# Kernel optimization log

Hardware: AMD Instinct MI355X
Metric: run time of the kernel (lower is better)

## Reference

```python
import jax, jax.numpy as jnp
import numpy as np

N_NODES = 100000


def setup_inputs() -> dict:
    key = jax.random.key(0)
    k1, k2, k3, k4, k5, k6 = jax.random.split(key, 6)
    n_edges = 1600000
    in_f, out_f = 64, 64
    x = jax.random.normal(k1, (N_NODES, in_f), dtype=jnp.float32)
    edge_row = jax.random.randint(k2, (n_edges,), 0, N_NODES, dtype=jnp.int32)
    edge_col = jax.random.randint(k3, (n_edges,), 0, N_NODES, dtype=jnp.int32)
    edge_val = jax.random.uniform(k4, (n_edges,), dtype=jnp.float32)
    stdv = 1.0 / np.sqrt(out_f)
    weight = jax.random.uniform(k5, (in_f, out_f), dtype=jnp.float32, minval=-stdv, maxval=stdv)
    bias = jax.random.uniform(k6, (out_f,), dtype=jnp.float32, minval=-stdv, maxval=stdv)
    return {"x": x, "edge_row": edge_row, "edge_col": edge_col,
            "edge_val": edge_val, "weight": weight, "bias": bias}


def reference(x, edge_row, edge_col, edge_val, weight, bias):
    # spmm: support[i] = sum_{e: row[e]==i} val[e] * x[col[e]]
    msgs = edge_val[:, None] * x[edge_col]              # [E, in_f]
    support = jax.ops.segment_sum(msgs, edge_row, num_segments=N_NODES)  # [N, in_f]
    out = support @ weight + bias                       # [N, out_f]
    # row-wise L2 normalize (no eps, matching torch.norm division)
    norm = jnp.linalg.norm(out, axis=1, keepdims=True)  # [N, 1]
    return out / norm
```

## Files before the change

kernel.cpp:

```cpp
#include <hip/hip_runtime.h>

#define N_NODES 100000
#define FDIM 64
#define BROWS 128
#define NBUCK ((N_NODES + BROWS - 1) / BROWS)
#define EDGES_PER_BLK 8192
#define BCAP 3072

#define WS_BBASE_OFF (656u * 1024u)
#define WS_BTOT_OFF  (672u * 1024u)
#define WS_CV_OFF    (1024u * 1024u)
#define WS_XH_OFF    (14u * 1024u * 1024u)

__device__ __forceinline__ unsigned short f2bf(float f) {
    unsigned int u = __float_as_uint(f);
    return (unsigned short)((u + 0x7FFFu + ((u >> 16) & 1u)) >> 16);
}
__device__ __forceinline__ float bf2f(unsigned short h) {
    return __uint_as_float((unsigned int)h << 16);
}

__global__ __launch_bounds__(256) void spmm_atomic(
    const float* __restrict__ x, const int* __restrict__ erow,
    const int* __restrict__ ecol, const float* __restrict__ eval,
    float* __restrict__ out, int n_edges)
{
    int tid = blockIdx.x * 256 + threadIdx.x;
    int e = tid >> 4, l = tid & 15;
    if (e >= n_edges) return;
    int row = erow[e], col = ecol[e];
    float v = eval[e];
    const float4 xv = *reinterpret_cast<const float4*>(x + (size_t)col * FDIM + l * 4);
    float* dst = out + (size_t)row * FDIM + l * 4;
    unsafeAtomicAdd(dst + 0, v * xv.x);
    unsafeAtomicAdd(dst + 1, v * xv.y);
    unsafeAtomicAdd(dst + 2, v * xv.z);
    unsafeAtomicAdd(dst + 3, v * xv.w);
}

__global__ __launch_bounds__(256) void gemm_xw(
    const float* __restrict__ x, const float* __restrict__ W,
    unsigned short* __restrict__ yh)
{
    __shared__ float4 Wl[64][16];
    __shared__ float  s[4][4][68];

    const int t = threadIdx.x;
    for (int i = t; i < 64 * 16; i += 256)
        ((float4*)Wl)[i] = ((const float4*)W)[i];

    const int wid  = t >> 6;
    const int lane = t & 63;
    const int sub  = lane >> 4;
    const int l    = lane & 15;
    const long base = (long)blockIdx.x * 16 + wid * 4;

    float4 sv = *reinterpret_cast<const float4*>(x + base * FDIM + lane * 4);
    *reinterpret_cast<float4*>(&s[wid][lane >> 4][(lane & 15) * 4]) = sv;
    __syncthreads();

    float4 acc = {0.f, 0.f, 0.f, 0.f};
    const float* srow = s[wid][sub];
    #pragma unroll
    for (int k = 0; k < FDIM; ++k) {
        const float a = srow[k];
        const float4 w = Wl[k][l];
        acc.x += a * w.x; acc.y += a * w.y; acc.z += a * w.z; acc.w += a * w.w;
    }
    ushort4 h;
    h.x = f2bf(acc.x); h.y = f2bf(acc.y); h.z = f2bf(acc.z); h.w = f2bf(acc.w);
    *reinterpret_cast<ushort4*>(yh + (size_t)(base + sub) * FDIM + l * 4) = h;
}

__global__ __launch_bounds__(1024) void count_blocks(
    const int* __restrict__ erow, int* __restrict__ cnts,
    int n_edges, int nblk)
{
    __shared__ int cnt[NBUCK];
    const int blk = blockIdx.x, t = threadIdx.x;
    for (int i = t; i < NBUCK; i += 1024) cnt[i] = 0;
    __syncthreads();
    const int beg = blk * EDGES_PER_BLK;
    const int end = min(beg + EDGES_PER_BLK, n_edges);
    for (int i = beg + t; i < end; i += 1024)
        atomicAdd(&cnt[erow[i] >> 7], 1);
    __syncthreads();
    for (int b = t; b < NBUCK; b += 1024)
        cnts[b * nblk + blk] = cnt[b];
}

__global__ __launch_bounds__(256) void scan_within_bucket(
    int* __restrict__ cnts, int* __restrict__ btot, int nblk)
{
    __shared__ int ssum[256];
    const int b = blockIdx.x, t = threadIdx.x;
    const int c = (t < nblk) ? cnts[b * nblk + t] : 0;
    ssum[t] = c;
    __syncthreads();
    for (int off = 1; off < 256; off <<= 1) {
        int v = (t >= off) ? ssum[t - off] : 0;
        __syncthreads();
        ssum[t] += v;
        __syncthreads();
    }
    if (t < nblk) cnts[b * nblk + t] = ssum[t] - c;
    if (t == 255) btot[b] = ssum[255];
}

__global__ __launch_bounds__(1024) void scan_btot(
    const int* __restrict__ btot, int* __restrict__ bbase, int n_edges)
{
    __shared__ int ssum[1024];
    const int t = threadIdx.x;
    const int v0 = (t < NBUCK) ? btot[t] : 0;
    ssum[t] = v0;
    __syncthreads();
    for (int off = 1; off < 1024; off <<= 1) {
        int v = (t >= off) ? ssum[t - off] : 0;
        __syncthreads();
        ssum[t] += v;
        __syncthreads();
    }
    if (t < NBUCK) bbase[t] = ssum[t] - v0;
    if (t == 0) bbase[NBUCK] = n_edges;
}

__global__ __launch_bounds__(1024) void bin_pass2(
    const int* __restrict__ erow, const int* __restrict__ ecol,
    const float* __restrict__ eval, const int* __restrict__ cnts,
    const int* __restrict__ bbase, int2* __restrict__ cvbin,
    int n_edges, int nblk)
{
    __shared__ int cur[NBUCK];
    const int blk = blockIdx.x, t = threadIdx.x;
    for (int b = t; b < NBUCK; b += 1024)
        cur[b] = bbase[b] + cnts[b * nblk + blk];
    __syncthreads();
    const int beg = blk * EDGES_PER_BLK;
    const int end = min(beg + EDGES_PER_BLK, n_edges);
    for (int i = beg + t; i < end; i += 1024) {
        int r = erow[i];
        int b = r >> 7;
        int pos = atomicAdd(&cur[b], 1);
        cvbin[pos] = make_int2(ecol[i] | ((r & 127) << 20), __float_as_int(eval[i]));
    }
}

__global__ __launch_bounds__(256) void sort_bucket(
    const int* __restrict__ bbase, int2* __restrict__ cvbin,
    int* __restrict__ endoff)
{
    __shared__ int2 se[BCAP];
    __shared__ int  hcnt[BROWS];
    __shared__ int  tmp[BROWS];
    __shared__ int  hoff[BROWS];
    const int b = blockIdx.x, t = threadIdx.x;
    const int beg = bbase[b];
    const int end = bbase[b + 1];
    const int n = end - beg;

    for (int i = t; i < n; i += 256) se[i] = cvbin[beg + i];
    if (t < BROWS) hcnt[t] = 0;
    __syncthreads();

    for (int i = t; i < n; i += 256) atomicAdd(&hcnt[se[i].x >> 20], 1);
    __syncthreads();

    if (t < BROWS) tmp[t] = hcnt[t];
    __syncthreads();
    for (int off = 1; off < BROWS; off <<= 1) {
        int val = (t < BROWS && t >= off) ? tmp[t - off] : 0;
        __syncthreads();
        if (t < BROWS) tmp[t] += val;
        __syncthreads();
    }
    if (t < BROWS) hoff[t] = tmp[t] - hcnt[t];
    __syncthreads();

    for (int i = t; i < n; i += 256) {
        int2 e = se[i];
        int pos = atomicAdd(&hoff[e.x >> 20], 1);
        cvbin[beg + pos] = e;
    }
    __syncthreads();

    if (t < BROWS) {
        int row = b * BROWS + t;
        if (row < N_NODES) endoff[row] = beg + hoff[t];
    }
}

__global__ __launch_bounds__(256) void spmm_csr(
    const float* __restrict__ x, const int* __restrict__ endoff,
    const int2* __restrict__ cv, float* __restrict__ out)
{
    const int wave = (blockIdx.x * 256 + threadIdx.x) >> 6;
    if (wave >= N_NODES) return;
    const int lane = threadIdx.x & 63;
    const int sub = lane >> 4, l = lane & 15;
    const int r = wave;
    const int beg = (r == 0) ? 0 : endoff[r - 1];
    const int end = endoff[r];

    float4 acc = {0.f, 0.f, 0.f, 0.f};
    int it = beg + sub;
    for (; it + 12 < end; it += 16) {
        const int2 ea = cv[it];
        const int2 eb = cv[it + 4];
        const int2 ec = cv[it + 8];
        const int2 ed = cv[it + 12];
        const float4 xa = *reinterpret_cast<const float4*>(x + (size_t)(ea.x & 0xFFFFF) * FDIM + l * 4);
        const float4 xb = *reinterpret_cast<const float4*>(x + (size_t)(eb.x & 0xFFFFF) * FDIM + l * 4);
        const float4 xc = *reinterpret_cast<const float4*>(x + (size_t)(ec.x & 0xFFFFF) * FDIM + l * 4);
        const float4 xd = *reinterpret_cast<const float4*>(x + (size_t)(ed.x & 0xFFFFF) * FDIM + l * 4);
        const float va = __int_as_float(ea.y);
        const float vb = __int_as_float(eb.y);
        const float vc = __int_as_float(ec.y);
        const float vd = __int_as_float(ed.y);
        acc.x += va * xa.x; acc.y += va * xa.y; acc.z += va * xa.z; acc.w += va * xa.w;
        acc.x += vb * xb.x; acc.y += vb * xb.y; acc.z += vb * xb.z; acc.w += vb * xb.w;
        acc.x += vc * xc.x; acc.y += vc * xc.y; acc.z += vc * xc.z; acc.w += vc * xc.w;
        acc.x += vd * xd.x; acc.y += vd * xd.y; acc.z += vd * xd.z; acc.w += vd * xd.w;
    }
    for (; it < end; it += 4) {
        const int2 e = cv[it];
        const float v = __int_as_float(e.y);
        const float4 xv = *reinterpret_cast<const float4*>(x + (size_t)(e.x & 0xFFFFF) * FDIM + l * 4);
        acc.x += v * xv.x; acc.y += v * xv.y; acc.z += v * xv.z; acc.w += v * xv.w;
    }
    #pragma unroll
    for (int off = 16; off < 64; off <<= 1) {
        acc.x += __shfl_xor(acc.x, off);
        acc.y += __shfl_xor(acc.y, off);
        acc.z += __shfl_xor(acc.z, off);
        acc.w += __shfl_xor(acc.w, off);
    }
    if (sub == 0)
        *reinterpret_cast<float4*>(out + (size_t)r * FDIM + l * 4) = acc;
}

__global__ __launch_bounds__(256) void spmm_fused(
    const unsigned short* __restrict__ yh, const int* __restrict__ endoff,
    const int2* __restrict__ cv, const float* __restrict__ bias,
    float* __restrict__ out)
{
    const int sg = (blockIdx.x * 256 + threadIdx.x) >> 4;
    if (sg >= N_NODES) return;
    const int l = threadIdx.x & 15;
    const int beg = (sg == 0) ? 0 : endoff[sg - 1];
    const int end = endoff[sg];

    float4 acc = {0.f, 0.f, 0.f, 0.f};
    int it = beg;
    for (; it + 3 < end; it += 4) {
        const int2 ea = cv[it];
        const int2 eb = cv[it + 1];
        const int2 ec = cv[it + 2];
        const int2 ed = cv[it + 3];
        const ushort4 xa = *reinterpret_cast<const ushort4*>(yh + (size_t)(ea.x & 0xFFFFF) * FDIM + l * 4);
        const ushort4 xb = *reinterpret_cast<const ushort4*>(yh + (size_t)(eb.x & 0xFFFFF) * FDIM + l * 4);
        const ushort4 xc = *reinterpret_cast<const ushort4*>(yh + (size_t)(ec.x & 0xFFFFF) * FDIM + l * 4);
        const ushort4 xd = *reinterpret_cast<const ushort4*>(yh + (size_t)(ed.x & 0xFFFFF) * FDIM + l * 4);
        const float va = __int_as_float(ea.y);
        const float vb = __int_as_float(eb.y);
        const float vc = __int_as_float(ec.y);
        const float vd = __int_as_float(ed.y);
        acc.x += va * bf2f(xa.x); acc.y += va * bf2f(xa.y); acc.z += va * bf2f(xa.z); acc.w += va * bf2f(xa.w);
        acc.x += vb * bf2f(xb.x); acc.y += vb * bf2f(xb.y); acc.z += vb * bf2f(xb.z); acc.w += vb * bf2f(xb.w);
        acc.x += vc * bf2f(xc.x); acc.y += vc * bf2f(xc.y); acc.z += vc * bf2f(xc.z); acc.w += vc * bf2f(xc.w);
        acc.x += vd * bf2f(xd.x); acc.y += vd * bf2f(xd.y); acc.z += vd * bf2f(xd.z); acc.w += vd * bf2f(xd.w);
    }
    for (; it < end; ++it) {
        const int2 e = cv[it];
        const float v = __int_as_float(e.y);
        const ushort4 xv = *reinterpret_cast<const ushort4*>(yh + (size_t)(e.x & 0xFFFFF) * FDIM + l * 4);
        acc.x += v * bf2f(xv.x); acc.y += v * bf2f(xv.y); acc.z += v * bf2f(xv.z); acc.w += v * bf2f(xv.w);
    }

    const float4 b = *reinterpret_cast<const float4*>(bias + l * 4);
    acc.x += b.x; acc.y += b.y; acc.z += b.z; acc.w += b.w;

    float p = acc.x * acc.x + acc.y * acc.y + acc.z * acc.z + acc.w * acc.w;
    #pragma unroll
    for (int off = 1; off < 16; off <<= 1)
        p += __shfl_xor(p, off);
    const float inv = 1.0f / sqrtf(p);
    acc.x *= inv; acc.y *= inv; acc.z *= inv; acc.w *= inv;

    *reinterpret_cast<float4*>(out + (size_t)sg * FDIM + l * 4) = acc;
}

__global__ __launch_bounds__(256) void gemm_norm(
    float* __restrict__ io, const float* __restrict__ W,
    const float* __restrict__ bias)
{
    __shared__ float4 Wl[64][16];
    __shared__ float4 bl[16];
    __shared__ float  s[4][4][68];

    const int t = threadIdx.x;
    for (int i = t; i < 64 * 16; i += 256)
        ((float4*)Wl)[i] = ((const float4*)W)[i];
    if (t < 16) bl[t] = ((const float4*)bias)[t];

    const int wid  = t >> 6;
    const int lane = t & 63;
    const int sub  = lane >> 4;
    const int l    = lane & 15;
    const long base = (long)blockIdx.x * 16 + wid * 4;

    float4 sv = *reinterpret_cast<const float4*>(io + base * FDIM + lane * 4);
    *reinterpret_cast<float4*>(&s[wid][lane >> 4][(lane & 15) * 4]) = sv;
    __syncthreads();

    float4 acc = {0.f, 0.f, 0.f, 0.f};
    const float* srow = s[wid][sub];
    #pragma unroll
    for (int k = 0; k < FDIM; ++k) {
        const float a = srow[k];
        const float4 w = Wl[k][l];
        acc.x += a * w.x; acc.y += a * w.y; acc.z += a * w.z; acc.w += a * w.w;
    }
    const float4 b = bl[l];
    acc.x += b.x; acc.y += b.y; acc.z += b.z; acc.w += b.w;

    float p = acc.x*acc.x + acc.y*acc.y + acc.z*acc.z + acc.w*acc.w;
    #pragma unroll
    for (int off = 1; off < 16; off <<= 1)
        p += __shfl_xor(p, off);
    const float inv = 1.0f / sqrtf(p);
    acc.x *= inv; acc.y *= inv; acc.z *= inv; acc.w *= inv;

    *reinterpret_cast<float4*>(io + (base + sub) * FDIM + l * 4) = acc;
}

extern "C" void kernel_launch(void* const* d_in, const int* in_sizes, int n_in,
                              void* d_out, int out_size, void* d_ws, size_t ws_size,
                              hipStream_t stream) {
    const float* x    = (const float*)d_in[0];
    const int*   erow = (const int*)d_in[1];
    const int*   ecol = (const int*)d_in[2];
    const float* eval = (const float*)d_in[3];
    const float* W    = (const float*)d_in[4];
    const float* bias = (const float*)d_in[5];
    float* out = (float*)d_out;
    const int n_edges = in_sizes[1];

    const int nblk = (n_edges + EDGES_PER_BLK - 1) / EDGES_PER_BLK;
    const size_t need = (size_t)WS_CV_OFF + (size_t)n_edges * sizeof(int2);
    const size_t need_bf16 = (size_t)WS_XH_OFF + (size_t)N_NODES * FDIM * sizeof(short);
    const bool cnts_fit =
        (size_t)NBUCK * nblk * sizeof(int) <= WS_BBASE_OFF && nblk <= 256;

    if (ws_size >= need && cnts_fit) {
        int*  cnts   = (int*)d_ws;
        int*  endoff = (int*)d_ws;
        int*  bbase  = (int*)((char*)d_ws + WS_BBASE_OFF);
        int*  btot   = (int*)((char*)d_ws + WS_BTOT_OFF);
        int2* cvbin  = (int2*)((char*)d_ws + WS_CV_OFF);
        unsigned short* yh = (unsigned short*)((char*)d_ws + WS_XH_OFF);
        const bool use_bf16 = (ws_size >= need_bf16);

        if (use_bf16)
            gemm_xw<<<N_NODES / 16, 256, 0, stream>>>(x, W, yh);
        count_blocks<<<nblk, 1024, 0, stream>>>(erow, cnts, n_edges, nblk);
        scan_within_bucket<<<NBUCK, 256, 0, stream>>>(cnts, btot, nblk);
        scan_btot<<<1, 1024, 0, stream>>>(btot, bbase, n_edges);
        bin_pass2<<<nblk, 1024, 0, stream>>>(erow, ecol, eval, cnts, bbase, cvbin,
                                             n_edges, nblk);
        sort_bucket<<<NBUCK, 256, 0, stream>>>(bbase, cvbin, endoff);
        if (use_bf16) {
            spmm_fused<<<((N_NODES * 16) + 255) / 256, 256, 0, stream>>>(
                yh, endoff, cvbin, bias, out);
        } else {
            spmm_csr<<<(N_NODES + 3) / 4, 256, 0, stream>>>(x, endoff, cvbin, out);
            gemm_norm<<<N_NODES / 16, 256, 0, stream>>>(out, W, bias);
        }
    } else {
        hipMemsetAsync(out, 0, (size_t)N_NODES * FDIM * sizeof(float), stream);
        long threads = (long)n_edges * 16;
        spmm_atomic<<<(int)((threads + 255) / 256), 256, 0, stream>>>(
            x, erow, ecol, eval, out, n_edges);
        gemm_norm<<<N_NODES / 16, 256, 0, stream>>>(out, W, bias);
    }
}
```

Before: 102.7 us.

## Fuse bucket sort into SpMM kernel with 64-row buckets held in LDS

Merges the per-bucket counting sort and the bf16 SpMM/bias/normalize kernel into one kernel. Each bucket's sorted edges stay in shared memory instead of being written back to global memory and reread, and the per-row end-offset array is dropped. Buckets shrink to 64 rows (BCAP 1536) and the edge-count blocks grow to 16384 edges, so scan_btot now handles two buckets per thread. A slow linear-scan fallback covers buckets that overflow shared memory, and occupancy and parallelism now depend on only 1563 blocks doing 4 rows per 16-lane group.

```diff
diff --git a/kernel.cpp b/kernel.cpp
--- a/kernel.cpp
+++ b/kernel.cpp
@@ -2,10 +2,10 @@
 
 #define N_NODES 100000
 #define FDIM 64
-#define BROWS 128
+#define BROWS 64
 #define NBUCK ((N_NODES + BROWS - 1) / BROWS)
-#define EDGES_PER_BLK 8192
-#define BCAP 3072
+#define EDGES_PER_BLK 16384
+#define BCAP 1536
 
 #define WS_BBASE_OFF (656u * 1024u)
 #define WS_BTOT_OFF  (672u * 1024u)
@@ -83,7 +83,7 @@
     const int beg = blk * EDGES_PER_BLK;
     const int end = min(beg + EDGES_PER_BLK, n_edges);
     for (int i = beg + t; i < end; i += 1024)
-        atomicAdd(&cnt[erow[i] >> 7], 1);
+        atomicAdd(&cnt[erow[i] >> 6], 1);
     __syncthreads();
     for (int b = t; b < NBUCK; b += 1024)
         cnts[b * nblk + blk] = cnt[b];
@@ -112,8 +112,11 @@
 {
     __shared__ int ssum[1024];
     const int t = threadIdx.x;
-    const int v0 = (t < NBUCK) ? btot[t] : 0;
-    ssum[t] = v0;
+    const int i0 = 2 * t, i1 = 2 * t + 1;
+    const int v0 = (i0 < NBUCK) ? btot[i0] : 0;
+    const int v1 = (i1 < NBUCK) ? btot[i1] : 0;
+    const int s = v0 + v1;
+    ssum[t] = s;
     __syncthreads();
     for (int off = 1; off < 1024; off <<= 1) {
         int v = (t >= off) ? ssum[t - off] : 0;
@@ -121,7 +124,9 @@
         ssum[t] += v;
         __syncthreads();
     }
-    if (t < NBUCK) bbase[t] = ssum[t] - v0;
+    int base = ssum[t] - s;
+    if (i0 < NBUCK) bbase[i0] = base;
+    if (i1 < NBUCK) bbase[i1] = base + v0;
     if (t == 0) bbase[NBUCK] = n_edges;
 }
 
@@ -140,154 +145,113 @@
     const int end = min(beg + EDGES_PER_BLK, n_edges);
     for (int i = beg + t; i < end; i += 1024) {
         int r = erow[i];
-        int b = r >> 7;
+        int b = r >> 6;
         int pos = atomicAdd(&cur[b], 1);
-        cvbin[pos] = make_int2(ecol[i] | ((r & 127) << 20), __float_as_int(eval[i]));
-    }
-}
-
-__global__ __launch_bounds__(256) void sort_bucket(
-    const int* __restrict__ bbase, int2* __restrict__ cvbin,
-    int* __restrict__ endoff)
+        cvbin[pos] = make_int2(ecol[i] | ((r & 63) << 20), __float_as_int(eval[i]));
+    }
+}
+
+__global__ __launch_bounds__(256) void sort_spmm(
+    const int* __restrict__ bbase, const int2* __restrict__ cvbin,
+    const unsigned short* __restrict__ yh, const float* __restrict__ bias,
+    float* __restrict__ out)
 {
     __shared__ int2 se[BCAP];
     __shared__ int  hcnt[BROWS];
-    __shared__ int  tmp[BROWS];
-    __shared__ int  hoff[BROWS];
+    __shared__ int  scn[BROWS];
+    __shared__ int  rowbeg[BROWS];
+    __shared__ int  cur[BROWS];
+
     const int b = blockIdx.x, t = threadIdx.x;
     const int beg = bbase[b];
     const int end = bbase[b + 1];
     const int n = end - beg;
-
-    for (int i = t; i < n; i += 256) se[i] = cvbin[beg + i];
+    const bool fits = (n <= BCAP);
+
     if (t < BROWS) hcnt[t] = 0;
     __syncthreads();
 
-    for (int i = t; i < n; i += 256) atomicAdd(&hcnt[se[i].x >> 20], 1);
-    __syncthreads();
-
-    if (t < BROWS) tmp[t] = hcnt[t];
-    __syncthreads();
-    for (int off = 1; off < BROWS; off <<= 1) {
-        int val = (t < BROWS && t >= off) ? tmp[t - off] : 0;
-        __syncthreads();
-        if (t < BROWS) tmp[t] += val;
-        __syncthreads();
-    }
-    if (t < BROWS) hoff[t] = tmp[t] - hcnt[t];
-    __syncthreads();
-
-    for (int i = t; i < n; i += 256) {
-        int2 e = se[i];
-        int pos = atomicAdd(&hoff[e.x >> 20], 1);
-        cvbin[beg + pos] = e;
-    }
-    __syncthreads();
-
-    if (t < BROWS) {
-        int row = b * BROWS + t;
-        if (row < N_NODES) endoff[row] = beg + hoff[t];
-    }
-}
-
-__global__ __launch_bounds__(256) void spmm_csr(
-    const float* __restrict__ x, const int* __restrict__ endoff,
-    const int2* __restrict__ cv, float* __restrict__ out)
-{
-    const int wave = (blockIdx.x * 256 + threadIdx.x) >> 6;
-    if (wave >= N_NODES) return;
-    const int lane = threadIdx.x & 63;
-    const int sub = lane >> 4, l = lane & 15;
-    const int r = wave;
-    const int beg = (r == 0) ? 0 : endoff[r - 1];
-    const int end = endoff[r];
-
-    float4 acc = {0.f, 0.f, 0.f, 0.f};
-    int it = beg + sub;
-    for (; it + 12 < end; it += 16) {
-        const int2 ea = cv[it];
-        const int2 eb = cv[it + 4];
-        const int2 ec = cv[it + 8];
-        const int2 ed = cv[it + 12];
-        const float4 xa = *reinterpret_cast<const float4*>(x + (size_t)(ea.x & 0xFFFFF) * FDIM + l * 4);
-        const float4 xb = *reinterpret_cast<const float4*>(x + (size_t)(eb.x & 0xFFFFF) * FDIM + l * 4);
-        const float4 xc = *reinterpret_cast<const float4*>(x + (size_t)(ec.x & 0xFFFFF) * FDIM + l * 4);
-        const float4 xd = *reinterpret_cast<const float4*>(x + (size_t)(ed.x & 0xFFFFF) * FDIM + l * 4);
-        const float va = __int_as_float(ea.y);
-        const float vb = __int_as_float(eb.y);
-        const float vc = __int_as_float(ec.y);
-        const float vd = __int_as_float(ed.y);
-        acc.x += va * xa.x; acc.y += va * xa.y; acc.z += va * xa.z; acc.w += va * xa.w;
-        acc.x += vb * xb.x; acc.y += vb * xb.y; acc.z += vb * xb.z; acc.w += vb * xb.w;
-        acc.x += vc * xc.x; acc.y += vc * xc.y; acc.z += vc * xc.z; acc.w += vc * xc.w;
-        acc.x += vd * xd.x; acc.y += vd * xd.y; acc.z += vd * xd.z; acc.w += vd * xd.w;
-    }
-    for (; it < end; it += 4) {
-        const int2 e = cv[it];
-        const float v = __int_as_float(e.y);
-        const float4 xv = *reinterpret_cast<const float4*>(x + (size_t)(e.x & 0xFFFFF) * FDIM + l * 4);
-        acc.x += v * xv.x; acc.y += v * xv.y; acc.z += v * xv.z; acc.w += v * xv.w;
-    }
+    if (fits) {
+        for (int i = t; i < n; i += 256)
+            atomicAdd(&hcnt[(cvbin[beg + i].x >> 20) & 63], 1);
+        __syncthreads();
+        if (t < BROWS) scn[t] = hcnt[t];
+        __syncthreads();
+        for (int off = 1; off < BROWS; off <<= 1) {
+            int v = (t < BROWS && t >= off) ? scn[t - off] : 0;
+            __syncthreads();
+            if (t < BROWS) scn[t] += v;
+            __syncthreads();
+        }
+        if (t < BROWS) { rowbeg[t] = scn[t] - hcnt[t]; cur[t] = scn[t] - hcnt[t]; }
+        __syncthreads();
+        for (int i = t; i < n; i += 256) {
+            int2 e = cvbin[beg + i];
+            int pos = atomicAdd(&cur[(e.x >> 20) & 63], 1);
+            se[pos] = e;
+        }
+        __syncthreads();
+    }
+
+    const int sg = t >> 4, l = t & 15;
     #pragma unroll
-    for (int off = 16; off < 64; off <<= 1) {
-        acc.x += __shfl_xor(acc.x, off);
-        acc.y += __shfl_xor(acc.y, off);
-        acc.z += __shfl_xor(acc.z, off);
-        acc.w += __shfl_xor(acc.w, off);
-    }
-    if (sub == 0)
-        *reinterpret_cast<float4*>(out + (size_t)r * FDIM + l * 4) = acc;
-}
-
-__global__ __launch_bounds__(256) void spmm_fused(
-    const unsigned short* __restrict__ yh, const int* __restrict__ endoff,
-    const int2* __restrict__ cv, const float* __restrict__ bias,
-    float* __restrict__ out)
-{
-    const int sg = (blockIdx.x * 256 + threadIdx.x) >> 4;
-    if (sg >= N_NODES) return;
-    const int l = threadIdx.x & 15;
-    const int beg = (sg == 0) ? 0 : endoff[sg - 1];
-    const int end = endoff[sg];
-
-    float4 acc = {0.f, 0.f, 0.f, 0.f};
-    int it = beg;
-    for (; it + 3 < end; it += 4) {
-        const int2 ea = cv[it];
-        const int2 eb = cv[it + 1];
-        const int2 ec = cv[it + 2];
-        const int2 ed = cv[it + 3];
-        const ushort4 xa = *reinterpret_cast<const ushort4*>(yh + (size_t)(ea.x & 0xFFFFF) * FDIM + l * 4);
-        const ushort4 xb = *reinterpret_cast<const ushort4*>(yh + (size_t)(eb.x & 0xFFFFF) * FDIM + l * 4);
-        const ushort4 xc = *reinterpret_cast<const ushort4*>(yh + (size_t)(ec.x & 0xFFFFF) * FDIM + l * 4);
-        const ushort4 xd = *reinterpret_cast<const ushort4*>(yh + (size_t)(ed.x & 0xFFFFF) * FDIM + l * 4);
-        const float va = __int_as_float(ea.y);
-        const float vb = __int_as_float(eb.y);
-        const float vc = __int_as_float(ec.y);
-        const float vd = __int_as_float(ed.y);
-        acc.x += va * bf2f(xa.x); acc.y += va * bf2f(xa.y); acc.z += va * bf2f(xa.z); acc.w += va * bf2f(xa.w);
-        acc.x += vb * bf2f(xb.x); acc.y += vb * bf2f(xb.y); acc.z += vb * bf2f(xb.z); acc.w += vb * bf2f(xb.w);
-        acc.x += vc * bf2f(xc.x); acc.y += vc * bf2f(xc.y); acc.z += vc * bf2f(xc.z); acc.w += vc * bf2f(xc.w);
-        acc.x += vd * bf2f(xd.x); acc.y += vd * bf2f(xd.y); acc.z += vd * bf2f(xd.z); acc.w += vd * bf2f(xd.w);
-    }
-    for (; it < end; ++it) {
-        const int2 e = cv[it];
-        const float v = __int_as_float(e.y);
-        const ushort4 xv = *reinterpret_cast<const ushort4*>(yh + (size_t)(e.x & 0xFFFFF) * FDIM + l * 4);
-        acc.x += v * bf2f(xv.x); acc.y += v * bf2f(xv.y); acc.z += v * bf2f(xv.z); acc.w += v * bf2f(xv.w);
-    }
-
-    const float4 b = *reinterpret_cast<const float4*>(bias + l * 4);
-    acc.x += b.x; acc.y += b.y; acc.z += b.z; acc.w += b.w;
-
-    float p = acc.x * acc.x + acc.y * acc.y + acc.z * acc.z + acc.w * acc.w;
-    #pragma unroll
-    for (int off = 1; off < 16; off <<= 1)
-        p += __shfl_xor(p, off);
-    const float inv = 1.0f / sqrtf(p);
-    acc.x *= inv; acc.y *= inv; acc.z *= inv; acc.w *= inv;
-
-    *reinterpret_cast<float4*>(out + (size_t)sg * FDIM + l * 4) = acc;
+    for (int rr = 0; rr < 4; ++rr) {
+        const int r = sg + 16 * rr;
+        const int row = b * BROWS + r;
+        float4 acc = {0.f, 0.f, 0.f, 0.f};
+
+        if (fits) {
+            const int rb = rowbeg[r];
+            const int re = rb + hcnt[r];
+            int it = rb;
+            for (; it + 3 < re; it += 4) {
+                const int2 ea = se[it];
+                const int2 eb = se[it + 1];
+                const int2 ec = se[it + 2];
+                const int2 ed = se[it + 3];
+                const ushort4 xa = *reinterpret_cast<const ushort4*>(yh + (size_t)(ea.x & 0xFFFFF) * FDIM + l * 4);
+                const ushort4 xb = *reinterpret_cast<const ushort4*>(yh + (size_t)(eb.x & 0xFFFFF) * FDIM + l * 4);
+                const ushort4 xc = *reinterpret_cast<const ushort4*>(yh + (size_t)(ec.x & 0xFFFFF) * FDIM + l * 4);
+                const ushort4 xd = *reinterpret_cast<const ushort4*>(yh + (size_t)(ed.x & 0xFFFFF) * FDIM + l * 4);
+                const float va = __int_as_float(ea.y);
+                const float vb = __int_as_float(eb.y);
+                const float vc = __int_as_float(ec.y);
+                const float vd = __int_as_float(ed.y);
+                acc.x += va * bf2f(xa.x); acc.y += va * bf2f(xa.y); acc.z += va * bf2f(xa.z); acc.w += va * bf2f(xa.w);
+                acc.x += vb * bf2f(xb.x); acc.y += vb * bf2f(xb.y); acc.z += vb * bf2f(xb.z); acc.w += vb * bf2f(xb.w);
+                acc.x += vc * bf2f(xc.x); acc.y += vc * bf2f(xc.y); acc.z += vc * bf2f(xc.z); acc.w += vc * bf2f(xc.w);
+                acc.x += vd * bf2f(xd.x); acc.y += vd * bf2f(xd.y); acc.z += vd * bf2f(xd.z); acc.w += vd * bf2f(xd.w);
+            }
+            for (; it < re; ++it) {
+                const int2 e = se[it];
+                const float v = __int_as_float(e.y);
+                const ushort4 xv = *reinterpret_cast<const ushort4*>(yh + (size_t)(e.x & 0xFFFFF) * FDIM + l * 4);
+                acc.x += v * bf2f(xv.x); acc.y += v * bf2f(xv.y); acc.z += v * bf2f(xv.z); acc.w += v * bf2f(xv.w);
+            }
+        } else {
+            for (int i = beg; i < end; ++i) {
+                const int2 e = cvbin[i];
+                if (((e.x >> 20) & 63) == r) {
+                    const float v = __int_as_float(e.y);
+                    const ushort4 xv = *reinterpret_cast<const ushort4*>(yh + (size_t)(e.x & 0xFFFFF) * FDIM + l * 4);
+                    acc.x += v * bf2f(xv.x); acc.y += v * bf2f(xv.y); acc.z += v * bf2f(xv.z); acc.w += v * bf2f(xv.w);
+                }
+            }
+        }
+
+        const float4 bv = *reinterpret_cast<const float4*>(bias + l * 4);
+        acc.x += bv.x; acc.y += bv.y; acc.z += bv.z; acc.w += bv.w;
+
+        float p = acc.x * acc.x + acc.y * acc.y + acc.z * acc.z + acc.w * acc.w;
+        #pragma unroll
+        for (int off = 1; off < 16; off <<= 1)
+            p += __shfl_xor(p, off);
+        const float inv = 1.0f / sqrtf(p);
+        acc.x *= inv; acc.y *= inv; acc.z *= inv; acc.w *= inv;
+
+        if (row < N_NODES)
+            *reinterpret_cast<float4*>(out + (size_t)row * FDIM + l * 4) = acc;
+    }
 }
 
 __global__ __launch_bounds__(256) void gemm_norm(
@@ -347,35 +311,24 @@
     const int n_edges = in_sizes[1];
 
     const int nblk = (n_edges + EDGES_PER_BLK - 1) / EDGES_PER_BLK;
-    const size_t need = (size_t)WS_CV_OFF + (size_t)n_edges * sizeof(int2);
     const size_t need_bf16 = (size_t)WS_XH_OFF + (size_t)N_NODES * FDIM * sizeof(short);
     const bool cnts_fit =
         (size_t)NBUCK * nblk * sizeof(int) <= WS_BBASE_OFF && nblk <= 256;
 
-    if (ws_size >= need && cnts_fit) {
+    if (ws_size >= need_bf16 && cnts_fit) {
         int*  cnts   = (int*)d_ws;
-        int*  endoff = (int*)d_ws;
         int*  bbase  = (int*)((char*)d_ws + WS_BBASE_OFF);
         int*  btot   = (int*)((char*)d_ws + WS_BTOT_OFF);
         int2* cvbin  = (int2*)((char*)d_ws + WS_CV_OFF);
         unsigned short* yh = (unsigned short*)((char*)d_ws + WS_XH_OFF);
-        const bool use_bf16 = (ws_size >= need_bf16);
-
-        if (use_bf16)
-            gemm_xw<<<N_NODES / 16, 256, 0, stream>>>(x, W, yh);
+
+        gemm_xw<<<N_NODES / 16, 256, 0, stream>>>(x, W, yh);
         count_blocks<<<nblk, 1024, 0, stream>>>(erow, cnts, n_edges, nblk);
         scan_within_bucket<<<NBUCK, 256, 0, stream>>>(cnts, btot, nblk);
         scan_btot<<<1, 1024, 0, stream>>>(btot, bbase, n_edges);
         bin_pass2<<<nblk, 1024, 0, stream>>>(erow, ecol, eval, cnts, bbase, cvbin,
                                              n_edges, nblk);
-        sort_bucket<<<NBUCK, 256, 0, stream>>>(bbase, cvbin, endoff);
-        if (use_bf16) {
-            spmm_fused<<<((N_NODES * 16) + 255) / 256, 256, 0, stream>>>(
-                yh, endoff, cvbin, bias, out);
-        } else {
-            spmm_csr<<<(N_NODES + 3) / 4, 256, 0, stream>>>(x, endoff, cvbin, out);
-            gemm_norm<<<N_NODES / 16, 256, 0, stream>>>(out, W, bias);
-        }
+        sort_spmm<<<NBUCK, 256, 0, stream>>>(bbase, cvbin, yh, bias, out);
     } else {
         hipMemsetAsync(out, 0, (size_t)N_NODES * FDIM * sizeof(float), stream);
         long threads = (long)n_edges * 16;
```

Result: faster. 100.6 us (-2.1%).
